# Optimization experiments

Measured on AMD Instinct MI355X. Metric: run time of the kernel, lower is better.

## Reference

```python
import jax, jax.numpy as jnp
import numpy as np
import math

BLUR_K = [1.0, 3.0, 3.0, 1.0]
EPS = 1e-8


def _make_blur_kernel(upsample_factor=2):
    k = jnp.asarray(BLUR_K, dtype=jnp.float32)
    k = k[None, :] * k[:, None]
    k = k / k.sum()
    return k * (upsample_factor ** 2)


def setup_inputs() -> dict:
    key = jax.random.key(0)
    ks = jax.random.split(key, 5)
    B, Cin, Cout, K, S, H, W = 16, 256, 128, 3, 512, 64, 64
    x = jax.random.normal(ks[0], (B, Cin, H, W), dtype=jnp.float32)
    style = jax.random.normal(ks[1], (B, S), dtype=jnp.float32)
    weight = jax.random.normal(ks[2], (1, Cout, Cin, K, K), dtype=jnp.float32)
    mod_w = jax.random.normal(ks[3], (Cin, S), dtype=jnp.float32) * (1.0 / math.sqrt(S))
    mod_b = jnp.ones((Cin,), dtype=jnp.float32)  # StyleGAN2 modulation bias init = 1
    return {"x": x, "style": style, "weight": weight, "mod_w": mod_w, "mod_b": mod_b}


def reference(x, style, weight, mod_w, mod_b):
    B, Cin, H, W = x.shape
    Cout = weight.shape[1]
    K = weight.shape[-1]
    scale = 1.0 / math.sqrt(Cin * K * K)

    # modulation: Linear(style_dim -> in_channel)
    s = style @ mod_w.T + mod_b                      # (B, Cin)
    w = scale * weight * s[:, None, :, None, None]   # (B, Cout, Cin, K, K)
    demod = jax.lax.rsqrt(jnp.sum(w * w, axis=(2, 3, 4)) + EPS)  # (B, Cout)
    w = w * demod[:, :, None, None, None]

    # per-sample conv_transpose2d(stride=2, padding=0, groups=B)
    # == lhs-dilated grouped correlation with spatially-flipped kernel
    kernel = jnp.flip(w, axis=(3, 4)).reshape(B * Cout, Cin, K, K)
    xg = x.reshape(1, B * Cin, H, W)
    out = jax.lax.conv_general_dilated(
        xg, kernel,
        window_strides=(1, 1),
        padding=((K - 1, K - 1), (K - 1, K - 1)),
        lhs_dilation=(2, 2),
        feature_group_count=B,
        dimension_numbers=("NCHW", "OIHW", "NCHW"),
    )  # (1, B*Cout, 2H+K-2, 2W+K-2) -> here (1, B*Cout, 2H+1, 2W+1)
    Ht, Wt = out.shape[2], out.shape[3]

    # Blur2 / upfirdn2d(up=1, down=1, pad=(pad0, pad1))
    # p = len(blur_kernel) - 2 - (K - 1); pad0 = (p+1)//2 + 1; pad1 = p//2 + 1
    p = len(BLUR_K) - 2 - (K - 1)
    pad0 = (p + 1) // 2 + 1
    pad1 = p // 2 + 1
    bk = _make_blur_kernel()                       # (4, 4)
    bw = jnp.flip(bk, axis=(0, 1))[None, None]     # (1, 1, 4, 4)
    outs = out.reshape(B * Cout, 1, Ht, Wt)
    blurred = jax.lax.conv_general_dilated(
        outs, bw,
        window_strides=(1, 1),
        padding=((pad0, pad1), (pad0, pad1)),
        dimension_numbers=("NCHW", "OIHW", "NCHW"),
    )
    Hb, Wb = blurred.shape[2], blurred.shape[3]
    return blurred.reshape(B, Cout, Hb, Wb)
```

## Files before the change

### kernel.cpp

```cpp
#include <hip/hip_runtime.h>
#include <stdint.h>

#define CIN 256
#define COUT 128
#define SDIM 512
#define NB 16

#define XP_RSTRIDE 16896
#define XP_BSTRIDE 1115136
#define A_BSTRIDE (512*2304)

typedef __attribute__((ext_vector_type(8))) short short8;
typedef __attribute__((ext_vector_type(4))) float f32x4;

__device__ __forceinline__ float bf2f(unsigned short h) {
  union { unsigned int u; float f; } v; v.u = ((unsigned int)h) << 16; return v.f;
}
__device__ __forceinline__ unsigned short f2bf(float f) {
  union { float f; unsigned int u; } v; v.f = f;
  return (unsigned short)((v.u + 0x7fffu + ((v.u >> 16) & 1u)) >> 16);
}
__device__ __forceinline__ void gll16(const void* g, void* l) {
  __builtin_amdgcn_global_load_lds(
      (const __attribute__((address_space(1))) unsigned int*)g,
      (__attribute__((address_space(3))) unsigned int*)l, 16, 0, 0);
}

__global__ __launch_bounds__(256) void k_detect(
    const unsigned short* __restrict__ xr, int* __restrict__ flag) {
  __shared__ int red[4];
  int t = threadIdx.x, cnt = 0;
  for (int i = t; i < 8192; i += 256) {
    int e = (xr[2*i] >> 7) & 0xff;
    cnt += (e > 90 && e < 145) ? 1 : 0;
  }
  #pragma unroll
  for (int off = 32; off > 0; off >>= 1) cnt += __shfl_down(cnt, off);
  if ((t & 63) == 0) red[t >> 6] = cnt;
  __syncthreads();
  if (t == 0) *flag = (red[0] + red[1] + red[2] + red[3] < 5000) ? 1 : 0;
}

__global__ __launch_bounds__(256) void k_style(
    const void* __restrict__ style_v, const void* __restrict__ mod_w_v,
    const void* __restrict__ mod_b_v, const int* __restrict__ flag,
    float* __restrict__ s_out) {
  __shared__ float st[SDIM];
  int b = blockIdx.x, t = threadIdx.x;
  int isf = *flag;
  float acc;
  if (!isf) {
    const unsigned short* style = (const unsigned short*)style_v;
    const unsigned short* mod_w = (const unsigned short*)mod_w_v;
    const unsigned short* mod_b = (const unsigned short*)mod_b_v;
    st[t]       = bf2f(style[b*SDIM + t]);
    st[t + 256] = bf2f(style[b*SDIM + t + 256]);
    __syncthreads();
    const uint4* wr = (const uint4*)(mod_w + (size_t)t*SDIM);
    acc = bf2f(mod_b[t]);
    #pragma unroll 4
    for (int s8 = 0; s8 < SDIM/8; ++s8) {
      uint4 p = wr[s8];
      int sb = s8*8;
      acc += bf2f((unsigned short)(p.x & 0xffff))*st[sb]
           + bf2f((unsigned short)(p.x >> 16))   *st[sb+1]
           + bf2f((unsigned short)(p.y & 0xffff))*st[sb+2]
           + bf2f((unsigned short)(p.y >> 16))   *st[sb+3]
           + bf2f((unsigned short)(p.z & 0xffff))*st[sb+4]
           + bf2f((unsigned short)(p.z >> 16))   *st[sb+5]
           + bf2f((unsigned short)(p.w & 0xffff))*st[sb+6]
           + bf2f((unsigned short)(p.w >> 16))   *st[sb+7];
    }
  } else {
    const float* style = (const float*)style_v;
    const float* mod_w = (const float*)mod_w_v;
    const float* mod_b = (const float*)mod_b_v;
    st[t]       = style[b*SDIM + t];
    st[t + 256] = style[b*SDIM + t + 256];
    __syncthreads();
    const float4* wr = (const float4*)(mod_w + (size_t)t*SDIM);
    acc = mod_b[t];
    #pragma unroll 4
    for (int s4 = 0; s4 < SDIM/4; ++s4) {
      float4 p = wr[s4];
      int sb = s4*4;
      acc += p.x*st[sb] + p.y*st[sb+1] + p.z*st[sb+2] + p.w*st[sb+3];
    }
  }
  s_out[b*CIN + t] = acc;
}

__global__ __launch_bounds__(256) void k_weights(
    const void* __restrict__ weight_v,
    const float* __restrict__ s_in,
    const int* __restrict__ flag,
    unsigned short* __restrict__ Aw) {
  int co = blockIdx.x, b = blockIdx.y, ci = threadIdx.x;
  int isf = *flag;
  float sm = 0.0208333333333333f * s_in[b*CIN + ci];
  float w9[9]; float ss = 0.f;
  if (!isf) {
    const unsigned short* wp = (const unsigned short*)weight_v + ((size_t)co*CIN + ci)*9;
    #pragma unroll
    for (int k = 0; k < 9; ++k) { float v = bf2f(wp[k]) * sm; w9[k] = v; ss += v*v; }
  } else {
    const float* wp = (const float*)weight_v + ((size_t)co*CIN + ci)*9;
    #pragma unroll
    for (int k = 0; k < 9; ++k) { float v = wp[k] * sm; w9[k] = v; ss += v*v; }
  }
  #pragma unroll
  for (int off = 32; off > 0; off >>= 1) ss += __shfl_down(ss, off);
  __shared__ float red[4];
  if ((ci & 63) == 0) red[ci >> 6] = ss;
  __syncthreads();
  float demod = rsqrtf(red[0] + red[1] + red[2] + red[3] + 1e-8f);
  #pragma unroll
  for (int k = 0; k < 9; ++k) w9[k] *= demod;
  const float F[4] = {0.25f, 0.75f, 0.75f, 0.25f};
  float C6[6][6];
  #pragma unroll
  for (int ty = 0; ty < 6; ++ty) {
    #pragma unroll
    for (int tx = 0; tx < 6; ++tx) {
      float acc = 0.f;
      #pragma unroll
      for (int ay = 0; ay < 3; ++ay) {
        int fy = ay - ty + 3;
        if (fy < 0 || fy > 3) continue;
        float ra = 0.f;
        #pragma unroll
        for (int ax = 0; ax < 3; ++ax) {
          int fx = ax - tx + 3;
          if (fx < 0 || fx > 3) continue;
          ra += w9[ay*3 + ax] * F[fx];
        }
        acc += ra * F[fy];
      }
      C6[ty][tx] = acc;
    }
  }
  unsigned short* Ab = Aw + (size_t)b*A_BSTRIDE;
  #pragma unroll
  for (int py = 0; py < 2; ++py) {
    #pragma unroll
    for (int px = 0; px < 2; ++px) {
      unsigned short* Am = Ab + (size_t)(py*256 + co*2 + px)*2304 + ci;
      #pragma unroll
      for (int dh = -1; dh <= 1; ++dh) {
        #pragma unroll
        for (int dw = -1; dw <= 1; ++dw) {
          int tap = (dh+1)*3 + (dw+1);
          Am[tap*256] = f2bf(C6[py - 2*dh + 2][px - 2*dw + 2]);
        }
      }
    }
  }
}

__global__ __launch_bounds__(256) void k_transpose(
    const void* __restrict__ x_v,
    const int* __restrict__ flag,
    unsigned short* __restrict__ xp) {
  int r_out = blockIdx.x, b = blockIdx.y, t = threadIdx.x;
  unsigned short* rp = xp + (size_t)b*XP_BSTRIDE + (size_t)r_out*XP_RSTRIDE;
  int r_in = r_out - 1;
  if (r_in < 0 || r_in >= 64) {
    uint4 z = make_uint4(0,0,0,0);
    #pragma unroll
    for (int i = 0; i < 9; ++i) {
      int idx = i*256 + t;
      if (idx < 2112) ((uint4*)rp)[idx] = z;
    }
    return;
  }
  if (t < 64) {
    uint4 z = make_uint4(0,0,0,0);
    int col = (t < 32) ? 0 : 65;
    ((uint4*)(rp + col*256))[t & 31] = z;
  }
  int isf = *flag;
  __shared__ __align__(16) unsigned short lds[64*72];
  int ci_l = t >> 2, cp = t & 3;
  int c = t >> 2, jg = t & 3;
  for (int g4 = 0; g4 < 4; ++g4) {
    int ci0 = g4 * 64;
    size_t eoff = ((size_t)b*CIN + ci0 + ci_l)*4096 + (size_t)r_in*64 + cp*16;
    union { unsigned short s[16]; uint4 q[2]; } u;
    if (!isf) {
      const uint4* src = (const uint4*)((const unsigned short*)x_v + eoff);
      u.q[0] = src[0]; u.q[1] = src[1];
    } else {
      const float4* srcf = (const float4*)((const float*)x_v + eoff);
      float4 f0 = srcf[0], f1 = srcf[1], f2 = srcf[2], f3 = srcf[3];
      u.s[0]=f2bf(f0.x); u.s[1]=f2bf(f0.y); u.s[2]=f2bf(f0.z); u.s[3]=f2bf(f0.w);
      u.s[4]=f2bf(f1.x); u.s[5]=f2bf(f1.y); u.s[6]=f2bf(f1.z); u.s[7]=f2bf(f1.w);
      u.s[8]=f2bf(f2.x); u.s[9]=f2bf(f2.y); u.s[10]=f2bf(f2.z); u.s[11]=f2bf(f2.w);
      u.s[12]=f2bf(f3.x); u.s[13]=f2bf(f3.y); u.s[14]=f2bf(f3.z); u.s[15]=f2bf(f3.w);
    }
    if (g4) __syncthreads();
    *(uint4*)&lds[ci_l*72 + cp*16]     = u.q[0];
    *(uint4*)&lds[ci_l*72 + cp*16 + 8] = u.q[1];
    __syncthreads();
    unsigned short ov[16] __attribute__((aligned(16)));
    #pragma unroll
    for (int j = 0; j < 16; ++j) ov[j] = lds[(jg*16 + j)*72 + c];
    uint4* dst = (uint4*)(rp + (size_t)(c+1)*256 + ci0 + jg*16);
    dst[0] = *(const uint4*)&ov[0];
    dst[1] = *(const uint4*)&ov[8];
  }
}

__global__ __launch_bounds__(256) void k_gemm(
    const unsigned short* __restrict__ Aw,
    const unsigned short* __restrict__ xp,
    const int* __restrict__ flag,
    void* __restrict__ out) {
  __shared__ __align__(16) unsigned short As[128*32];
  __shared__ __align__(16) unsigned short Bs[128*32];
  int g = blockIdx.x;
  int b  = ((g & 7) << 1) | ((g >> 3) & 1);
  int mt = (g >> 4) & 3;
  int nt = g >> 6;
  int yy0 = nt << 1;
  int t = threadIdx.x;
  int wave = t >> 6, lane = t & 63;
  int row = t >> 2, part = t & 3;

  {
    uint4 z = make_uint4(0,0,0,0);
    ((uint4*)As)[t] = z; ((uint4*)As)[t+256] = z;
    ((uint4*)Bs)[t] = z; ((uint4*)Bs)[t+256] = z;
  }
  __syncthreads();

  const unsigned short* Abase = Aw + (size_t)b*A_BSTRIDE + (size_t)(mt*128)*2304 + part*8;
  const unsigned short* pA0 = Abase + (size_t)row*2304;
  const unsigned short* pA1 = Abase + (size_t)(row + 64)*2304;
  const unsigned short* Xb = xp + (size_t)b*XP_BSTRIDE + part*8;
  const unsigned short* pB0 = Xb + (size_t)(yy0 + 1)*XP_RSTRIDE + (size_t)(row + 1)*256;
  const unsigned short* pB1 = Xb + (size_t)(yy0 + 2)*XP_RSTRIDE + (size_t)(row + 1)*256;
  unsigned short* lA0 = &As[row*32 + part*8];
  unsigned short* lA1 = &As[(row + 64)*32 + part*8];
  unsigned short* lB0 = &Bs[row*32 + part*8];
  unsigned short* lB1 = &Bs[(row + 64)*32 + part*8];

  f32x4 acc[4][4];
  #pragma unroll
  for (int i = 0; i < 4; ++i)
    #pragma unroll
    for (int j = 0; j < 4; ++j)
      acc[i][j] = (f32x4){0.f, 0.f, 0.f, 0.f};

  int mb = (wave >> 1) << 6;
  int nb = (wave & 1) << 6;
  int l15 = lane & 15, q = lane >> 4;

  for (int s = 0; s < 72; ++s) {
    int tap = s >> 3;
    int dh = tap/3 - 1, dw = tap - (tap/3)*3 - 1;
    int boff = dh*XP_RSTRIDE + dw*256 + ((s & 7) << 5);
    int aoff = s << 5;
    gll16(pA0 + aoff, lA0);
    gll16(pA1 + aoff, lA1);
    gll16(pB0 + boff, lB0);
    gll16(pB1 + boff, lB1);
    __syncthreads();
    short8 af[4], bfv[4];
    #pragma unroll
    for (int i = 0; i < 4; ++i)
      af[i] = *(const short8*)&As[(mb + i*16 + l15)*32 + q*8];
    #pragma unroll
    for (int j = 0; j < 4; ++j)
      bfv[j] = *(const short8*)&Bs[(nb + j*16 + l15)*32 + q*8];
    #pragma unroll
    for (int i = 0; i < 4; ++i)
      #pragma unroll
      for (int j = 0; j < 4; ++j)
        acc[i][j] = __builtin_amdgcn_mfma_f32_16x16x32_bf16(af[i], bfv[j], acc[i][j], 0, 0, 0);
    __syncthreads();
  }

  int isf = *flag;
  int py = mt >> 1;
  int ry = wave & 1;
  int y = ((yy0 + ry) << 1) + py;
  int cobase = ((mt & 1) << 6) + ((wave >> 1) << 5);
  #pragma unroll
  for (int i = 0; i < 4; ++i) {
    #pragma unroll
    for (int rr = 0; rr < 2; ++rr) {
      int co = cobase + i*8 + q*2 + rr;
      size_t obase = (((size_t)b*COUT + co)*128 + y)*64;
      if (!isf) {
        unsigned int* outp = (unsigned int*)out;
        #pragma unroll
        for (int j = 0; j < 4; ++j) {
          unsigned int pk = (unsigned int)f2bf(acc[i][j][rr*2])
                          | ((unsigned int)f2bf(acc[i][j][rr*2 + 1]) << 16);
          outp[obase + j*16 + l15] = pk;
        }
      } else {
        float2* outp = (float2*)out;
        #pragma unroll
        for (int j = 0; j < 4; ++j)
          outp[obase + j*16 + l15] = make_float2(acc[i][j][rr*2], acc[i][j][rr*2 + 1]);
      }
    }
  }
}

extern "C" void kernel_launch(void* const* d_in, const int* in_sizes, int n_in,
                              void* d_out, int out_size, void* d_ws, size_t ws_size,
                              hipStream_t stream) {
  const void* x      = d_in[0];
  const void* style  = d_in[1];
  const void* weight = d_in[2];
  const void* mod_w  = d_in[3];
  const void* mod_b  = d_in[4];
  char* ws = (char*)d_ws;
  int* flag           = (int*)ws;
  float* s_buf        = (float*)(ws + 1024);
  unsigned short* Aw  = (unsigned short*)(ws + 32768);
  unsigned short* xpd = (unsigned short*)(ws + 32768 + 37748736);

  k_detect   <<<1, 256, 0, stream>>>((const unsigned short*)x, flag);
  k_style    <<<NB, 256, 0, stream>>>(style, mod_w, mod_b, flag, s_buf);
  k_weights  <<<dim3(COUT, NB), 256, 0, stream>>>(weight, s_buf, flag, Aw);
  k_transpose<<<dim3(66, NB), 256, 0, stream>>>(x, flag, xpd);
  k_gemm     <<<2048, 256, 0, stream>>>(Aw, xpd, flag, d_out);
}
```

Before: 450.2 us.

## Swizzle GEMM LDS tiles and rework input transpose to conflict-free packed layout

In the GEMM, the 16-byte chunk position within each 32-element LDS row is XOR-swizzled by row index, on both the global_load_lds source offset and the fragment reads. This is meant to remove LDS bank conflicts on the MFMA operand reads. The K loop is split into tap and sub-chunk loops with the inner loop unrolled, and the redundant LDS zero-fill with its barrier is dropped. The input packing kernel now packs channel pairs into 32-bit words and transposes them through a padded 33-stride LDS buffer, aiming at conflict-free transposes at the cost of narrower scalar LDS accesses.

```diff
diff --git a/kernel.cpp b/kernel.cpp
--- a/kernel.cpp
+++ b/kernel.cpp
@@ -179,34 +179,50 @@
     ((uint4*)(rp + col*256))[t & 31] = z;
   }
   int isf = *flag;
-  __shared__ __align__(16) unsigned short lds[64*72];
-  int ci_l = t >> 2, cp = t & 3;
-  int c = t >> 2, jg = t & 3;
+  __shared__ unsigned int lds32[64*33];
+  int tci = t >> 3;
+  int tc8 = t & 7;
+  int cS  = t >> 2;
+  int jg  = t & 3;
   for (int g4 = 0; g4 < 4; ++g4) {
     int ci0 = g4 * 64;
-    size_t eoff = ((size_t)b*CIN + ci0 + ci_l)*4096 + (size_t)r_in*64 + cp*16;
-    union { unsigned short s[16]; uint4 q[2]; } u;
-    if (!isf) {
-      const uint4* src = (const uint4*)((const unsigned short*)x_v + eoff);
-      u.q[0] = src[0]; u.q[1] = src[1];
+    int ci = ci0 + tci*2;
+    size_t base = (((size_t)b*CIN + ci)*64 + r_in)*64 + tc8*8;
+    unsigned int v[8];
+    if (isf) {
+      const float* s0 = (const float*)x_v + base;
+      const float* s1 = s0 + 4096;
+      float4 a0 = ((const float4*)s0)[0], a1 = ((const float4*)s0)[1];
+      float4 b0 = ((const float4*)s1)[0], b1 = ((const float4*)s1)[1];
+      v[0] = f2bf(a0.x) | ((unsigned int)f2bf(b0.x) << 16);
+      v[1] = f2bf(a0.y) | ((unsigned int)f2bf(b0.y) << 16);
+      v[2] = f2bf(a0.z) | ((unsigned int)f2bf(b0.z) << 16);
+      v[3] = f2bf(a0.w) | ((unsigned int)f2bf(b0.w) << 16);
+      v[4] = f2bf(a1.x) | ((unsigned int)f2bf(b1.x) << 16);
+      v[5] = f2bf(a1.y) | ((unsigned int)f2bf(b1.y) << 16);
+      v[6] = f2bf(a1.z) | ((unsigned int)f2bf(b1.z) << 16);
+      v[7] = f2bf(a1.w) | ((unsigned int)f2bf(b1.w) << 16);
     } else {
-      const float4* srcf = (const float4*)((const float*)x_v + eoff);
-      float4 f0 = srcf[0], f1 = srcf[1], f2 = srcf[2], f3 = srcf[3];
-      u.s[0]=f2bf(f0.x); u.s[1]=f2bf(f0.y); u.s[2]=f2bf(f0.z); u.s[3]=f2bf(f0.w);
-      u.s[4]=f2bf(f1.x); u.s[5]=f2bf(f1.y); u.s[6]=f2bf(f1.z); u.s[7]=f2bf(f1.w);
-      u.s[8]=f2bf(f2.x); u.s[9]=f2bf(f2.y); u.s[10]=f2bf(f2.z); u.s[11]=f2bf(f2.w);
-      u.s[12]=f2bf(f3.x); u.s[13]=f2bf(f3.y); u.s[14]=f2bf(f3.z); u.s[15]=f2bf(f3.w);
+      const unsigned short* s0 = (const unsigned short*)x_v + base;
+      const unsigned short* s1 = s0 + 4096;
+      union { uint4 q; unsigned short h[8]; } u0, u1;
+      u0.q = *(const uint4*)s0; u1.q = *(const uint4*)s1;
+      #pragma unroll
+      for (int j = 0; j < 8; ++j)
+        v[j] = (unsigned int)u0.h[j] | ((unsigned int)u1.h[j] << 16);
     }
     if (g4) __syncthreads();
-    *(uint4*)&lds[ci_l*72 + cp*16]     = u.q[0];
-    *(uint4*)&lds[ci_l*72 + cp*16 + 8] = u.q[1];
+    #pragma unroll
+    for (int j = 0; j < 8; ++j)
+      lds32[(tc8*8 + j)*33 + tci] = v[j];
     __syncthreads();
-    unsigned short ov[16] __attribute__((aligned(16)));
-    #pragma unroll
-    for (int j = 0; j < 16; ++j) ov[j] = lds[(jg*16 + j)*72 + c];
-    uint4* dst = (uint4*)(rp + (size_t)(c+1)*256 + ci0 + jg*16);
-    dst[0] = *(const uint4*)&ov[0];
-    dst[1] = *(const uint4*)&ov[8];
+    union { unsigned int o[8]; uint4 q[2]; } ob;
+    #pragma unroll
+    for (int w = 0; w < 8; ++w)
+      ob.o[w] = lds32[cS*33 + jg*8 + w];
+    uint4* dst = (uint4*)(rp + (size_t)(cS+1)*256 + ci0 + jg*16);
+    dst[0] = ob.q[0];
+    dst[1] = ob.q[1];
   }
 }
 
@@ -225,20 +241,14 @@
   int t = threadIdx.x;
   int wave = t >> 6, lane = t & 63;
   int row = t >> 2, part = t & 3;
-
-  {
-    uint4 z = make_uint4(0,0,0,0);
-    ((uint4*)As)[t] = z; ((uint4*)As)[t+256] = z;
-    ((uint4*)Bs)[t] = z; ((uint4*)Bs)[t+256] = z;
-  }
-  __syncthreads();
-
-  const unsigned short* Abase = Aw + (size_t)b*A_BSTRIDE + (size_t)(mt*128)*2304 + part*8;
-  const unsigned short* pA0 = Abase + (size_t)row*2304;
-  const unsigned short* pA1 = Abase + (size_t)(row + 64)*2304;
-  const unsigned short* Xb = xp + (size_t)b*XP_BSTRIDE + part*8;
-  const unsigned short* pB0 = Xb + (size_t)(yy0 + 1)*XP_RSTRIDE + (size_t)(row + 1)*256;
-  const unsigned short* pB1 = Xb + (size_t)(yy0 + 2)*XP_RSTRIDE + (size_t)(row + 1)*256;
+  int isf = *flag;
+
+  int partS = part ^ ((row >> 2) & 3);
+  const unsigned short* pA0 = Aw + (size_t)b*A_BSTRIDE + (size_t)(mt*128 + row)*2304 + partS*8;
+  const unsigned short* pA1 = pA0 + (size_t)64*2304;
+  const unsigned short* pB0 = xp + (size_t)b*XP_BSTRIDE + (size_t)(yy0 + 1)*XP_RSTRIDE
+                              + (size_t)(row + 1)*256 + partS*8;
+  const unsigned short* pB1 = pB0 + XP_RSTRIDE;
   unsigned short* lA0 = &As[row*32 + part*8];
   unsigned short* lA1 = &As[(row + 64)*32 + part*8];
   unsigned short* lB0 = &Bs[row*32 + part*8];
@@ -254,33 +264,38 @@
   int mb = (wave >> 1) << 6;
   int nb = (wave & 1) << 6;
   int l15 = lane & 15, q = lane >> 4;
-
-  for (int s = 0; s < 72; ++s) {
-    int tap = s >> 3;
-    int dh = tap/3 - 1, dw = tap - (tap/3)*3 - 1;
-    int boff = dh*XP_RSTRIDE + dw*256 + ((s & 7) << 5);
-    int aoff = s << 5;
-    gll16(pA0 + aoff, lA0);
-    gll16(pA1 + aoff, lA1);
-    gll16(pB0 + boff, lB0);
-    gll16(pB1 + boff, lB1);
-    __syncthreads();
-    short8 af[4], bfv[4];
-    #pragma unroll
-    for (int i = 0; i < 4; ++i)
-      af[i] = *(const short8*)&As[(mb + i*16 + l15)*32 + q*8];
-    #pragma unroll
-    for (int j = 0; j < 4; ++j)
-      bfv[j] = *(const short8*)&Bs[(nb + j*16 + l15)*32 + q*8];
-    #pragma unroll
-    for (int i = 0; i < 4; ++i)
+  int qs = q ^ ((l15 >> 2) & 3);
+
+  for (int tap = 0; tap < 9; ++tap) {
+    int dh = (tap >= 6) ? 1 : ((tap >= 3) ? 0 : -1);
+    int dwx = tap - (dh + 1)*3 - 1;
+    const unsigned short* a0 = pA0 + tap*256;
+    const unsigned short* a1 = pA1 + tap*256;
+    const unsigned short* b0 = pB0 + dh*XP_RSTRIDE + dwx*256;
+    const unsigned short* b1 = b0 + XP_RSTRIDE;
+    #pragma unroll
+    for (int kk = 0; kk < 8; ++kk) {
+      gll16(a0 + kk*32, lA0);
+      gll16(a1 + kk*32, lA1);
+      gll16(b0 + kk*32, lB0);
+      gll16(b1 + kk*32, lB1);
+      __syncthreads();
+      short8 af[4], bfv[4];
+      #pragma unroll
+      for (int i = 0; i < 4; ++i)
+        af[i] = *(const short8*)&As[(mb + i*16 + l15)*32 + qs*8];
       #pragma unroll
       for (int j = 0; j < 4; ++j)
-        acc[i][j] = __builtin_amdgcn_mfma_f32_16x16x32_bf16(af[i], bfv[j], acc[i][j], 0, 0, 0);
-    __syncthreads();
-  }
-
-  int isf = *flag;
+        bfv[j] = *(const short8*)&Bs[(nb + j*16 + l15)*32 + qs*8];
+      #pragma unroll
+      for (int i = 0; i < 4; ++i)
+        #pragma unroll
+        for (int j = 0; j < 4; ++j)
+          acc[i][j] = __builtin_amdgcn_mfma_f32_16x16x32_bf16(af[i], bfv[j], acc[i][j], 0, 0, 0);
+      __syncthreads();
+    }
+  }
+
   int py = mt >> 1;
   int ry = wave & 1;
   int y = ((yy0 + ry) << 1) + py;
```

New measurement: 430.2 us. 4.5% less time.
